# Optimization experiments

Hardware: AMD Instinct MI355X
Metric: run time of the kernel (lower is better)

The kernel has to match this reference:

```python
import jax, jax.numpy as jnp
import numpy as np
from jax import lax

B, C, O, H, W = 4, 96, 96, 128, 128
K = 3      # kernel size everywhere
D = 2      # dilation of dconv
KK = K * K


def conv2d(x, w, b, pad, dil=1):
    # x: [B,C,H,W], w: [O,C,K,K]
    y = lax.conv_general_dilated(
        x, w, window_strides=(1, 1), padding=[(pad, pad), (pad, pad)],
        rhs_dilation=(dil, dil), dimension_numbers=('NCHW', 'OIHW', 'NCHW'))
    return y + b[None, :, None, None]


def bilinear_sample(img, py, px):
    # img: [B,C,H,W]; py,px: [B,KK,H,W] float sample coords (zero outside)
    y0 = jnp.floor(py)
    x0 = jnp.floor(px)
    wy = py - y0
    wx = px - x0
    flat = img.reshape(B, 1, C, H * W)  # broadcast over KK

    def gather(yi, xi):
        valid = (yi >= 0) & (yi < H) & (xi >= 0) & (xi < W)
        yc = jnp.clip(yi, 0, H - 1).astype(jnp.int32)
        xc = jnp.clip(xi, 0, W - 1).astype(jnp.int32)
        idx = (yc * W + xc).reshape(B, KK, 1, H * W)
        g = jnp.take_along_axis(flat, idx, axis=3)  # [B,KK,C,H*W]
        g = g.reshape(B, KK, C, H, W)
        return g * valid.reshape(B, KK, 1, H, W)

    v00 = gather(y0, x0)
    v01 = gather(y0, x0 + 1)
    v10 = gather(y0 + 1, x0)
    v11 = gather(y0 + 1, x0 + 1)
    wy = wy[:, :, None]
    wx = wx[:, :, None]
    return ((1 - wy) * ((1 - wx) * v00 + wx * v01)
            + wy * ((1 - wx) * v10 + wx * v11))


def setup_inputs() -> dict:
    key = jax.random.key(0)
    ks = jax.random.split(key, 7)
    x = jax.random.normal(ks[0], (B, C, H, W), jnp.float32)
    s = 1.0 / np.sqrt(C * K * K)  # torch default conv init bound
    u = lambda k, shape: jax.random.uniform(k, shape, jnp.float32, -s, s)
    return dict(
        x=x,
        dconv_w=u(ks[1], (O, C, K, K)), dconv_b=u(ks[2], (O,)),
        off_w=u(ks[3], (2 * KK, C, K, K)), off_b=u(ks[4], (2 * KK,)),
        def_w=u(ks[5], (O, C, K, K)), def_b=u(ks[6], (O,)),
    )


def reference(x, dconv_w, dconv_b, off_w, off_b, def_w, def_b):
    # dilated conv + relu + residual (self.conv is unused in the original forward)
    x1 = conv2d(x, dconv_w, dconv_b, pad=D, dil=D)
    x3 = x + jax.nn.relu(x1)

    # offset prediction: [B, 2*KK, H, W] -> (dy, dx) per kernel tap
    offset = conv2d(x3, off_w, off_b, pad=1)
    off = offset.reshape(B, KK, 2, H, W)
    dy, dx = off[:, :, 0], off[:, :, 1]

    # base sampling grid: output pixel + kernel tap - padding
    ki, kj = jnp.meshgrid(jnp.arange(K), jnp.arange(K), indexing='ij')
    ky = (ki.reshape(-1) - (K - 1) // 2).astype(jnp.float32)  # [KK]
    kx = (kj.reshape(-1) - (K - 1) // 2).astype(jnp.float32)
    ygrid = jnp.arange(H, dtype=jnp.float32)[:, None]
    xgrid = jnp.arange(W, dtype=jnp.float32)[None, :]
    py = ygrid[None, None] + ky[None, :, None, None] + dy  # [B,KK,H,W]
    px = xgrid[None, None] + kx[None, :, None, None] + dx

    sampled = bilinear_sample(x3, py, px)  # [B,KK,C,H,W]
    out = jnp.einsum('bkchw,ock->bohw', sampled, def_w.reshape(O, C, KK))
    return out + def_b[None, :, None, None]
```

## Files before the change

### kernel.cpp

```cpp
#include <hip/hip_runtime.h>
#include <hip/hip_bf16.h>

#define BD 4
#define CD 96
#define OD 96
#define HD 128
#define WD 128
#define HWD (HD*WD)

typedef __attribute__((ext_vector_type(8))) short bfrag;
typedef __attribute__((ext_vector_type(4))) float ffrag;

__device__ __forceinline__ short f2bs(float f) {
    __hip_bfloat16 h = __float2bfloat16(f);
    return *reinterpret_cast<short*>(&h);
}

__device__ __forceinline__ int swizzle512(int gid) {
    return ((gid & 7) << 6) | (gid >> 3);
}

__global__ __launch_bounds__(256) void k_transpose(const float* __restrict__ x,
                                                   short* __restrict__ xb16) {
    __shared__ short tile[256 * 104];
    int pix0 = blockIdx.x * 256;
    int b = pix0 / HWD; int hw0 = pix0 % HWD;
    int tid = threadIdx.x;

    for (int e = tid; e < 96*64; e += 256) {
        int c = e >> 6, g = e & 63;
        float4 v = *(const float4*)(x + ((size_t)(b*96 + c))*HWD + hw0 + 4*g);
        tile[(4*g+0)*104 + c] = f2bs(v.x);
        tile[(4*g+1)*104 + c] = f2bs(v.y);
        tile[(4*g+2)*104 + c] = f2bs(v.z);
        tile[(4*g+3)*104 + c] = f2bs(v.w);
    }
    __syncthreads();
    for (int e = tid; e < 256*12; e += 256) {
        int px = e / 12, c8 = e % 12;
        bfrag v = *(const bfrag*)(tile + px*104 + c8*8);
        *(bfrag*)(xb16 + ((size_t)(pix0 + px))*96 + c8*8) = v;
    }
}

__global__ void k_repack(const float* __restrict__ dconv_w,
                         const float* __restrict__ off_w,
                         const float* __restrict__ def_w,
                         short* __restrict__ wB1,
                         short* __restrict__ wB2,
                         short* __restrict__ wB) {
    int t = blockIdx.x * blockDim.x + threadIdx.x;
    if (t < 27648) {
        int j = t & 7; int l = (t >> 3) & 63; int tile = t >> 9;
        int s = tile >> 1, nt = tile & 1;
        int k = 32*s + (l >> 4)*8 + j;
        int o = 16*nt + (l & 15);
        int c = k % 96, tap = k / 96;
        wB2[t] = (o < 18) ? f2bs(off_w[(o*96 + c)*9 + tap]) : (short)0;
    }
    if (t < 82944) {
        int j = t & 7; int l = (t >> 3) & 63; int tile = t >> 9;
        int s = tile / 6, nt = tile % 6;
        int k = 32*s + (l >> 4)*8 + j;
        int o = 16*nt + (l & 15);
        int c = k % 96, tap = k / 96;
        wB1[t] = f2bs(dconv_w[(o*96 + c)*9 + tap]);
        wB[t]  = f2bs(def_w [(o*96 + c)*9 + tap]);
    }
}

__global__ __launch_bounds__(256, 2) void k_conv1(const float* __restrict__ x,
                                                  const short* __restrict__ xb16,
                                                  const short* __restrict__ wB,
                                                  const float* __restrict__ bias,
                                                  short* __restrict__ x3b) {
    int pix0 = swizzle512(blockIdx.x) * 128;
    int b = pix0 / HWD; int hw0 = pix0 % HWD;
    int h = hw0 / WD;
    int tid = threadIdx.x;
    int l = tid & 63, wv = tid >> 6;
    int q = l >> 4, mr = l & 15;
    int wq = 32*wv;
    const short* xb = xb16 + ((size_t)b * HWD) * 96;
    const bfrag az = {0,0,0,0,0,0,0,0};

    ffrag acc[2][6];
    #pragma unroll
    for (int mt = 0; mt < 2; mt++)
        #pragma unroll
        for (int nt = 0; nt < 6; nt++) acc[mt][nt] = ffrag{0.f,0.f,0.f,0.f};

    #pragma unroll 1
    for (int tap = 0; tap < 9; tap++) {
        int y = h + (tap/3)*2 - 2;
        if ((unsigned)y >= HD) continue;
        const short* abase[2]; bool vx[2];
        #pragma unroll
        for (int mt = 0; mt < 2; mt++) {
            int xx = wq + 16*mt + mr + (tap%3)*2 - 2;
            int xxc = min(max(xx, 0), WD-1);
            vx[mt] = (unsigned)xx < WD;
            abase[mt] = xb + ((size_t)(y*WD + xxc))*96 + q*8;
        }
        #pragma unroll
        for (int sc = 0; sc < 3; sc++) {
            const short* wb = wB + ((size_t)((tap*3+sc)*6)*64 + l)*8;
            bfrag bb[6];
            #pragma unroll
            for (int nt = 0; nt < 6; nt++) bb[nt] = *(const bfrag*)(wb + nt*512);
            #pragma unroll
            for (int mt = 0; mt < 2; mt++) {
                bfrag a = *(const bfrag*)(abase[mt] + sc*32);
                if (!vx[mt]) a = az;
                #pragma unroll
                for (int nt = 0; nt < 6; nt++)
                    acc[mt][nt] = __builtin_amdgcn_mfma_f32_16x16x32_bf16(a, bb[nt], acc[mt][nt], 0, 0, 0);
            }
        }
    }

    #pragma unroll
    for (int mt = 0; mt < 2; mt++) {
        int hwb = hw0 + wq + 16*mt + q*4;
        #pragma unroll
        for (int nt = 0; nt < 6; nt++) {
            int o = 16*nt + mr;
            float bo = bias[o];
            float4 xr = *(const float4*)(x + ((size_t)(b*96 + o))*HWD + hwb);
            short* op = x3b + ((size_t)(b*HWD + hwb))*96 + o;
            op[0]   = f2bs(xr.x + fmaxf(acc[mt][nt][0] + bo, 0.f));
            op[96]  = f2bs(xr.y + fmaxf(acc[mt][nt][1] + bo, 0.f));
            op[192] = f2bs(xr.z + fmaxf(acc[mt][nt][2] + bo, 0.f));
            op[288] = f2bs(xr.w + fmaxf(acc[mt][nt][3] + bo, 0.f));
        }
    }
}

__global__ __launch_bounds__(256, 2) void k_deform(const short* __restrict__ x3b,
                                                   const short* __restrict__ wB2,
                                                   const float* __restrict__ off_b,
                                                   const short* __restrict__ wB,
                                                   const float* __restrict__ def_b,
                                                   float* __restrict__ out) {
    __shared__ float offsb[128][20];

    int pix0 = swizzle512(blockIdx.x) * 128;
    int b = pix0 / HWD; int hw0 = pix0 % HWD;
    int h = hw0 / WD;
    int tid = threadIdx.x;
    int l = tid & 63, wv = tid >> 6;
    int q = l >> 4, mr = l & 15;
    int wq = 32*wv;
    const short* xb = x3b + ((size_t)b * HWD) * 96;
    const bfrag az = {0,0,0,0,0,0,0,0};

    ffrag oa[2][2];
    #pragma unroll
    for (int mt = 0; mt < 2; mt++)
        #pragma unroll
        for (int nt = 0; nt < 2; nt++) oa[mt][nt] = ffrag{0.f,0.f,0.f,0.f};

    #pragma unroll 1
    for (int tap = 0; tap < 9; tap++) {
        int y = h + tap/3 - 1;
        if ((unsigned)y >= HD) continue;
        const short* abase[2]; bool vx[2];
        #pragma unroll
        for (int mt = 0; mt < 2; mt++) {
            int xx = wq + 16*mt + mr + tap%3 - 1;
            int xxc = min(max(xx, 0), WD-1);
            vx[mt] = (unsigned)xx < WD;
            abase[mt] = xb + ((size_t)(y*WD + xxc))*96 + q*8;
        }
        #pragma unroll
        for (int sc = 0; sc < 3; sc++) {
            const short* wb = wB2 + ((size_t)((tap*3+sc)*2)*64 + l)*8;
            bfrag b0 = *(const bfrag*)(wb);
            bfrag b1 = *(const bfrag*)(wb + 512);
            #pragma unroll
            for (int mt = 0; mt < 2; mt++) {
                bfrag a = *(const bfrag*)(abase[mt] + sc*32);
                if (!vx[mt]) a = az;
                oa[mt][0] = __builtin_amdgcn_mfma_f32_16x16x32_bf16(a, b0, oa[mt][0], 0, 0, 0);
                oa[mt][1] = __builtin_amdgcn_mfma_f32_16x16x32_bf16(a, b1, oa[mt][1], 0, 0, 0);
            }
        }
    }
    #pragma unroll
    for (int mt = 0; mt < 2; mt++) {
        int row = wq + 16*mt + q*4;
        float bo0 = off_b[mr];
        #pragma unroll
        for (int r = 0; r < 4; r++) offsb[row + r][mr] = oa[mt][0][r] + bo0;
        if (mr < 2) {
            float bo1 = off_b[16 + mr];
            #pragma unroll
            for (int r = 0; r < 4; r++) offsb[row + r][16 + mr] = oa[mt][1][r] + bo1;
        }
    }

    ffrag acc[2][6];
    #pragma unroll
    for (int mt = 0; mt < 2; mt++)
        #pragma unroll
        for (int nt = 0; nt < 6; nt++) acc[mt][nt] = ffrag{0.f,0.f,0.f,0.f};

    #pragma unroll 1
    for (int tap = 0; tap < 9; tap++) {
        const short* pp[2][4];
        float fb[2][4];
        #pragma unroll
        for (int mt = 0; mt < 2; mt++) {
            int w = wq + 16*mt + mr;
            float dy = offsb[w][2*tap];
            float dx = offsb[w][2*tap + 1];
            float py  = (float)(h + tap/3 - 1) + dy;
            float pxf = (float)(w + tap%3 - 1) + dx;
            float y0f = floorf(py), x0f = floorf(pxf);
            float wy = py - y0f, wx = pxf - x0f;
            int y0 = (int)y0f, x0 = (int)x0f;
            int y1 = y0 + 1, x1 = x0 + 1;
            bool vy0 = (unsigned)y0 < HD, vy1 = (unsigned)y1 < HD;
            bool vx0 = (unsigned)x0 < WD, vx1 = (unsigned)x1 < WD;
            fb[mt][0] = (vy0 && vx0) ? (1.f-wy)*(1.f-wx) : 0.f;
            fb[mt][1] = (vy0 && vx1) ? (1.f-wy)*wx       : 0.f;
            fb[mt][2] = (vy1 && vx0) ? wy*(1.f-wx)       : 0.f;
            fb[mt][3] = (vy1 && vx1) ? wy*wx             : 0.f;
            int yc0 = min(max(y0,0),HD-1), yc1 = min(max(y1,0),HD-1);
            int xc0 = min(max(x0,0),WD-1), xc1 = min(max(x1,0),WD-1);
            pp[mt][0] = xb + ((size_t)(yc0*WD + xc0))*96 + q*8;
            pp[mt][1] = xb + ((size_t)(yc0*WD + xc1))*96 + q*8;
            pp[mt][2] = xb + ((size_t)(yc1*WD + xc0))*96 + q*8;
            pp[mt][3] = xb + ((size_t)(yc1*WD + xc1))*96 + q*8;
        }
        #pragma unroll
        for (int sc = 0; sc < 3; sc++) {
            int s = tap*3 + sc;
            const short* wb = wB + ((size_t)(s*6)*64 + l)*8;
            bfrag bbf[6];
            #pragma unroll
            for (int nt = 0; nt < 6; nt++) bbf[nt] = *(const bfrag*)(wb + nt*512);
            #pragma unroll
            for (int mt = 0; mt < 2; mt++) {
                bfrag c00 = *(const bfrag*)(pp[mt][0] + sc*32);
                bfrag c01 = *(const bfrag*)(pp[mt][1] + sc*32);
                bfrag c10 = *(const bfrag*)(pp[mt][2] + sc*32);
                bfrag c11 = *(const bfrag*)(pp[mt][3] + sc*32);
                const int* i00 = (const int*)&c00;
                const int* i01 = (const int*)&c01;
                const int* i10 = (const int*)&c10;
                const int* i11 = (const int*)&c11;
                float f00 = fb[mt][0], f01 = fb[mt][1];
                float f10 = fb[mt][2], f11 = fb[mt][3];
                int ap[4];
                #pragma unroll
                for (int d = 0; d < 4; d++) {
                    float a0 = __int_as_float(((unsigned)i00[d]) << 16);
                    float b0f = __int_as_float(((unsigned)i01[d]) << 16);
                    float c0f = __int_as_float(((unsigned)i10[d]) << 16);
                    float d0 = __int_as_float(((unsigned)i11[d]) << 16);
                    float a1 = __int_as_float(i00[d] & 0xffff0000);
                    float b1f = __int_as_float(i01[d] & 0xffff0000);
                    float c1f = __int_as_float(i10[d] & 0xffff0000);
                    float d1 = __int_as_float(i11[d] & 0xffff0000);
                    float rlo = f00*a0 + f01*b0f + f10*c0f + f11*d0;
                    float rhi = f00*a1 + f01*b1f + f10*c1f + f11*d1;
                    ap[d] = (int)((unsigned short)f2bs(rlo)) |
                            ((int)((unsigned short)f2bs(rhi)) << 16);
                }
                bfrag a = *(const bfrag*)ap;
                #pragma unroll
                for (int nt = 0; nt < 6; nt++)
                    acc[mt][nt] = __builtin_amdgcn_mfma_f32_16x16x32_bf16(a, bbf[nt], acc[mt][nt], 0, 0, 0);
            }
        }
    }

    #pragma unroll
    for (int mt = 0; mt < 2; mt++) {
        int hwb = hw0 + wq + 16*mt + q*4;
        #pragma unroll
        for (int nt = 0; nt < 6; nt++) {
            int o = 16*nt + mr;
            float bo = def_b[o];
            float4 v;
            v.x = acc[mt][nt][0] + bo; v.y = acc[mt][nt][1] + bo;
            v.z = acc[mt][nt][2] + bo; v.w = acc[mt][nt][3] + bo;
            *(float4*)(out + ((size_t)(b*96 + o))*HWD + hwb) = v;
        }
    }
}

extern "C" void kernel_launch(void* const* d_in, const int* in_sizes, int n_in,
                              void* d_out, int out_size, void* d_ws, size_t ws_size,
                              hipStream_t stream) {
    const float* x       = (const float*)d_in[0];
    const float* dconv_w = (const float*)d_in[1];
    const float* dconv_b = (const float*)d_in[2];
    const float* off_w   = (const float*)d_in[3];
    const float* off_b   = (const float*)d_in[4];
    const float* def_w   = (const float*)d_in[5];
    const float* def_b   = (const float*)d_in[6];
    float* out = (float*)d_out;

    char* ws = (char*)d_ws;
    short* xb16 = (short*)(ws);
    short* x3b  = (short*)(ws + 12582912);
    short* wB1  = (short*)(ws + 25165824);
    short* wB2  = (short*)(ws + 25331712);
    short* wB   = (short*)(ws + 25387008);

    k_repack<<<324, 256, 0, stream>>>(dconv_w, off_w, def_w, wB1, wB2, wB);
    k_transpose<<<(BD*HWD)/256, 256, 0, stream>>>(x, xb16);
    k_conv1<<<(BD*HWD)/128, 256, 0, stream>>>(x, xb16, wB1, dconv_b, x3b);
    k_deform<<<(BD*HWD)/128, 256, 0, stream>>>(x3b, wB2, off_b, wB, def_b, out);
}
```

Baseline: 173.7 us.

## Software-pipeline gathers and weight loads in conv kernels; merge prep kernels

The tap/channel-chunk loops in the dilated-conv, offset-conv and deformable-conv stages are flattened into a single 27-step loop. It double-buffers the A fragments (including the four bilinear corners) and the B weight fragments, so loads for step s+1 are issued before the MFMAs of step s. Address and weight computation for the next tap is hoisted one step ahead. The transpose and weight-repack kernels are also merged into one launch. The pipelining raises register pressure and could lower occupancy under the 2-waves launch bound, and row-invalid taps are now computed with zeroed inputs instead of being skipped.

```diff
diff --git a/kernel.cpp b/kernel.cpp
--- a/kernel.cpp
+++ b/kernel.cpp
@@ -20,52 +20,52 @@
     return ((gid & 7) << 6) | (gid >> 3);
 }
 
-__global__ __launch_bounds__(256) void k_transpose(const float* __restrict__ x,
-                                                   short* __restrict__ xb16) {
+__global__ __launch_bounds__(256) void k_prep(const float* __restrict__ x,
+                                              const float* __restrict__ dconv_w,
+                                              const float* __restrict__ off_w,
+                                              const float* __restrict__ def_w,
+                                              short* __restrict__ xb16,
+                                              short* __restrict__ wB1,
+                                              short* __restrict__ wB2,
+                                              short* __restrict__ wB) {
     __shared__ short tile[256 * 104];
-    int pix0 = blockIdx.x * 256;
-    int b = pix0 / HWD; int hw0 = pix0 % HWD;
     int tid = threadIdx.x;
-
-    for (int e = tid; e < 96*64; e += 256) {
-        int c = e >> 6, g = e & 63;
-        float4 v = *(const float4*)(x + ((size_t)(b*96 + c))*HWD + hw0 + 4*g);
-        tile[(4*g+0)*104 + c] = f2bs(v.x);
-        tile[(4*g+1)*104 + c] = f2bs(v.y);
-        tile[(4*g+2)*104 + c] = f2bs(v.z);
-        tile[(4*g+3)*104 + c] = f2bs(v.w);
-    }
-    __syncthreads();
-    for (int e = tid; e < 256*12; e += 256) {
-        int px = e / 12, c8 = e % 12;
-        bfrag v = *(const bfrag*)(tile + px*104 + c8*8);
-        *(bfrag*)(xb16 + ((size_t)(pix0 + px))*96 + c8*8) = v;
-    }
-}
-
-__global__ void k_repack(const float* __restrict__ dconv_w,
-                         const float* __restrict__ off_w,
-                         const float* __restrict__ def_w,
-                         short* __restrict__ wB1,
-                         short* __restrict__ wB2,
-                         short* __restrict__ wB) {
-    int t = blockIdx.x * blockDim.x + threadIdx.x;
-    if (t < 27648) {
-        int j = t & 7; int l = (t >> 3) & 63; int tile = t >> 9;
-        int s = tile >> 1, nt = tile & 1;
-        int k = 32*s + (l >> 4)*8 + j;
-        int o = 16*nt + (l & 15);
-        int c = k % 96, tap = k / 96;
-        wB2[t] = (o < 18) ? f2bs(off_w[(o*96 + c)*9 + tap]) : (short)0;
-    }
-    if (t < 82944) {
-        int j = t & 7; int l = (t >> 3) & 63; int tile = t >> 9;
-        int s = tile / 6, nt = tile % 6;
-        int k = 32*s + (l >> 4)*8 + j;
-        int o = 16*nt + (l & 15);
-        int c = k % 96, tap = k / 96;
-        wB1[t] = f2bs(dconv_w[(o*96 + c)*9 + tap]);
-        wB[t]  = f2bs(def_w [(o*96 + c)*9 + tap]);
+    if (blockIdx.x < 256) {
+        int pix0 = blockIdx.x * 256;
+        int b = pix0 / HWD; int hw0 = pix0 % HWD;
+        for (int e = tid; e < 96*64; e += 256) {
+            int c = e >> 6, g = e & 63;
+            float4 v = *(const float4*)(x + ((size_t)(b*96 + c))*HWD + hw0 + 4*g);
+            tile[(4*g+0)*104 + c] = f2bs(v.x);
+            tile[(4*g+1)*104 + c] = f2bs(v.y);
+            tile[(4*g+2)*104 + c] = f2bs(v.z);
+            tile[(4*g+3)*104 + c] = f2bs(v.w);
+        }
+        __syncthreads();
+        for (int e = tid; e < 256*12; e += 256) {
+            int px = e / 12, c8 = e % 12;
+            bfrag v = *(const bfrag*)(tile + px*104 + c8*8);
+            *(bfrag*)(xb16 + ((size_t)(pix0 + px))*96 + c8*8) = v;
+        }
+    } else {
+        int t = (blockIdx.x - 256) * 256 + tid;
+        if (t < 27648) {
+            int j = t & 7; int l = (t >> 3) & 63; int tl = t >> 9;
+            int s = tl >> 1, nt = tl & 1;
+            int k = 32*s + (l >> 4)*8 + j;
+            int o = 16*nt + (l & 15);
+            int c = k % 96, tap = k / 96;
+            wB2[t] = (o < 18) ? f2bs(off_w[(o*96 + c)*9 + tap]) : (short)0;
+        }
+        if (t < 82944) {
+            int j = t & 7; int l = (t >> 3) & 63; int tl = t >> 9;
+            int s = tl / 6, nt = tl % 6;
+            int k = 32*s + (l >> 4)*8 + j;
+            int o = 16*nt + (l & 15);
+            int c = k % 96, tap = k / 96;
+            wB1[t] = f2bs(dconv_w[(o*96 + c)*9 + tap]);
+            wB[t]  = f2bs(def_w [(o*96 + c)*9 + tap]);
+        }
     }
 }
 
@@ -84,38 +84,64 @@
     const short* xb = xb16 + ((size_t)b * HWD) * 96;
     const bfrag az = {0,0,0,0,0,0,0,0};
 
+    auto aoff = [&](int tap, int mt, bool* vv) -> int {
+        int ty = tap/3, tx = tap - 3*(tap/3);
+        int y  = h + ty*2 - 2;
+        int xx = wq + 16*mt + mr + tx*2 - 2;
+        bool vy = (unsigned)y < HD, vx = (unsigned)xx < WD;
+        *vv = vy && vx;
+        int yc = min(max(y,0),HD-1), xc = min(max(xx,0),WD-1);
+        return (yc*WD + xc)*96 + q*8;
+    };
+
     ffrag acc[2][6];
     #pragma unroll
     for (int mt = 0; mt < 2; mt++)
         #pragma unroll
         for (int nt = 0; nt < 6; nt++) acc[mt][nt] = ffrag{0.f,0.f,0.f,0.f};
 
-    #pragma unroll 1
-    for (int tap = 0; tap < 9; tap++) {
-        int y = h + (tap/3)*2 - 2;
-        if ((unsigned)y >= HD) continue;
-        const short* abase[2]; bool vx[2];
+    int aoC[2], aoN[2]; bool vC[2], vN[2];
+    bfrag gA[2], gIn[2], bA[6], bIn[6];
+
+    #pragma unroll
+    for (int mt = 0; mt < 2; mt++) aoC[mt] = aoff(0, mt, &vC[mt]);
+    #pragma unroll
+    for (int mt = 0; mt < 2; mt++) gA[mt] = *(const bfrag*)(xb + aoC[mt]);
+    #pragma unroll
+    for (int nt = 0; nt < 6; nt++) bA[nt] = *(const bfrag*)(wB + ((size_t)nt*64 + l)*8);
+
+    #pragma unroll 3
+    for (int s = 0; s < 27; s++) {
+        int tap = s / 3, sc = s - 3*tap;
+        if (sc == 0) {
+            int tn = tap + 1; if (tn > 8) tn = 8;
+            #pragma unroll
+            for (int mt = 0; mt < 2; mt++) aoN[mt] = aoff(tn, mt, &vN[mt]);
+        }
         #pragma unroll
         for (int mt = 0; mt < 2; mt++) {
-            int xx = wq + 16*mt + mr + (tap%3)*2 - 2;
-            int xxc = min(max(xx, 0), WD-1);
-            vx[mt] = (unsigned)xx < WD;
-            abase[mt] = xb + ((size_t)(y*WD + xxc))*96 + q*8;
-        }
-        #pragma unroll
-        for (int sc = 0; sc < 3; sc++) {
-            const short* wb = wB + ((size_t)((tap*3+sc)*6)*64 + l)*8;
-            bfrag bb[6];
-            #pragma unroll
-            for (int nt = 0; nt < 6; nt++) bb[nt] = *(const bfrag*)(wb + nt*512);
-            #pragma unroll
-            for (int mt = 0; mt < 2; mt++) {
-                bfrag a = *(const bfrag*)(abase[mt] + sc*32);
-                if (!vx[mt]) a = az;
-                #pragma unroll
-                for (int nt = 0; nt < 6; nt++)
-                    acc[mt][nt] = __builtin_amdgcn_mfma_f32_16x16x32_bf16(a, bb[nt], acc[mt][nt], 0, 0, 0);
-            }
+            int off = (sc < 2) ? (aoC[mt] + (sc+1)*32) : aoN[mt];
+            gIn[mt] = *(const bfrag*)(xb + off);
+        }
+        int sn = s + 1; if (sn > 26) sn = 26;
+        #pragma unroll
+        for (int nt = 0; nt < 6; nt++)
+            bIn[nt] = *(const bfrag*)(wB + ((size_t)(sn*6 + nt)*64 + l)*8);
+        #pragma unroll
+        for (int mt = 0; mt < 2; mt++) {
+            bfrag a = gA[mt];
+            if (!vC[mt]) a = az;
+            #pragma unroll
+            for (int nt = 0; nt < 6; nt++)
+                acc[mt][nt] = __builtin_amdgcn_mfma_f32_16x16x32_bf16(a, bA[nt], acc[mt][nt], 0, 0, 0);
+        }
+        #pragma unroll
+        for (int mt = 0; mt < 2; mt++) gA[mt] = gIn[mt];
+        #pragma unroll
+        for (int nt = 0; nt < 6; nt++) bA[nt] = bIn[nt];
+        if (sc == 2) {
+            #pragma unroll
+            for (int mt = 0; mt < 2; mt++) { aoC[mt] = aoN[mt]; vC[mt] = vN[mt]; }
         }
     }
 
@@ -154,125 +180,194 @@
     const short* xb = x3b + ((size_t)b * HWD) * 96;
     const bfrag az = {0,0,0,0,0,0,0,0};
 
-    ffrag oa[2][2];
+    {
+        auto aoff2 = [&](int tap, int mt, bool* vv) -> int {
+            int ty = tap/3, tx = tap - 3*(tap/3);
+            int y  = h + ty - 1;
+            int xx = wq + 16*mt + mr + tx - 1;
+            bool vy = (unsigned)y < HD, vx = (unsigned)xx < WD;
+            *vv = vy && vx;
+            int yc = min(max(y,0),HD-1), xc = min(max(xx,0),WD-1);
+            return (yc*WD + xc)*96 + q*8;
+        };
+
+        ffrag oa[2][2];
+        #pragma unroll
+        for (int mt = 0; mt < 2; mt++)
+            #pragma unroll
+            for (int nt = 0; nt < 2; nt++) oa[mt][nt] = ffrag{0.f,0.f,0.f,0.f};
+
+        int aoC[2], aoN[2]; bool vC[2], vN[2];
+        bfrag gA[2], gIn[2], bA[2], bIn[2];
+
+        #pragma unroll
+        for (int mt = 0; mt < 2; mt++) aoC[mt] = aoff2(0, mt, &vC[mt]);
+        #pragma unroll
+        for (int mt = 0; mt < 2; mt++) gA[mt] = *(const bfrag*)(xb + aoC[mt]);
+        #pragma unroll
+        for (int nt = 0; nt < 2; nt++) bA[nt] = *(const bfrag*)(wB2 + ((size_t)nt*64 + l)*8);
+
+        #pragma unroll 3
+        for (int s = 0; s < 27; s++) {
+            int tap = s / 3, sc = s - 3*tap;
+            if (sc == 0) {
+                int tn = tap + 1; if (tn > 8) tn = 8;
+                #pragma unroll
+                for (int mt = 0; mt < 2; mt++) aoN[mt] = aoff2(tn, mt, &vN[mt]);
+            }
+            #pragma unroll
+            for (int mt = 0; mt < 2; mt++) {
+                int off = (sc < 2) ? (aoC[mt] + (sc+1)*32) : aoN[mt];
+                gIn[mt] = *(const bfrag*)(xb + off);
+            }
+            int sn = s + 1; if (sn > 26) sn = 26;
+            #pragma unroll
+            for (int nt = 0; nt < 2; nt++)
+                bIn[nt] = *(const bfrag*)(wB2 + ((size_t)(sn*2 + nt)*64 + l)*8);
+            #pragma unroll
+            for (int mt = 0; mt < 2; mt++) {
+                bfrag a = gA[mt];
+                if (!vC[mt]) a = az;
+                oa[mt][0] = __builtin_amdgcn_mfma_f32_16x16x32_bf16(a, bA[0], oa[mt][0], 0, 0, 0);
+                oa[mt][1] = __builtin_amdgcn_mfma_f32_16x16x32_bf16(a, bA[1], oa[mt][1], 0, 0, 0);
+            }
+            #pragma unroll
+            for (int mt = 0; mt < 2; mt++) gA[mt] = gIn[mt];
+            #pragma unroll
+            for (int nt = 0; nt < 2; nt++) bA[nt] = bIn[nt];
+            if (sc == 2) {
+                #pragma unroll
+                for (int mt = 0; mt < 2; mt++) { aoC[mt] = aoN[mt]; vC[mt] = vN[mt]; }
+            }
+        }
+        #pragma unroll
+        for (int mt = 0; mt < 2; mt++) {
+            int row = wq + 16*mt + q*4;
+            float bo0 = off_b[mr];
+            #pragma unroll
+            for (int r = 0; r < 4; r++) offsb[row + r][mr] = oa[mt][0][r] + bo0;
+            if (mr < 2) {
+                float bo1 = off_b[16 + mr];
+                #pragma unroll
+                for (int r = 0; r < 4; r++) offsb[row + r][16 + mr] = oa[mt][1][r] + bo1;
+            }
+        }
+    }
+
+    auto mkptr = [&](int tap, float dy, float dx, int wp, float* fo, int* oo) {
+        int ty = tap/3, tx = tap - 3*(tap/3);
+        float py  = (float)(h + ty - 1) + dy;
+        float pxf = (float)(wp + tx - 1) + dx;
+        float y0f = floorf(py), x0f = floorf(pxf);
+        float wy = py - y0f, wx = pxf - x0f;
+        int y0 = (int)y0f, x0 = (int)x0f;
+        int y1 = y0 + 1, x1 = x0 + 1;
+        bool vy0 = (unsigned)y0 < HD, vy1 = (unsigned)y1 < HD;
+        bool vx0 = (unsigned)x0 < WD, vx1 = (unsigned)x1 < WD;
+        fo[0] = (vy0 && vx0) ? (1.f-wy)*(1.f-wx) : 0.f;
+        fo[1] = (vy0 && vx1) ? (1.f-wy)*wx       : 0.f;
+        fo[2] = (vy1 && vx0) ? wy*(1.f-wx)       : 0.f;
+        fo[3] = (vy1 && vx1) ? wy*wx             : 0.f;
+        int yc0 = min(max(y0,0),HD-1), yc1 = min(max(y1,0),HD-1);
+        int xc0 = min(max(x0,0),WD-1), xc1 = min(max(x1,0),WD-1);
+        oo[0] = (yc0*WD + xc0)*96 + q*8;
+        oo[1] = (yc0*WD + xc1)*96 + q*8;
+        oo[2] = (yc1*WD + xc0)*96 + q*8;
+        oo[3] = (yc1*WD + xc1)*96 + q*8;
+    };
+
+    ffrag acc[2][6];
     #pragma unroll
     for (int mt = 0; mt < 2; mt++)
         #pragma unroll
-        for (int nt = 0; nt < 2; nt++) oa[mt][nt] = ffrag{0.f,0.f,0.f,0.f};
-
-    #pragma unroll 1
-    for (int tap = 0; tap < 9; tap++) {
-        int y = h + tap/3 - 1;
-        if ((unsigned)y >= HD) continue;
-        const short* abase[2]; bool vx[2];
+        for (int nt = 0; nt < 6; nt++) acc[mt][nt] = ffrag{0.f,0.f,0.f,0.f};
+
+    float fbv[2][4], fbn[2][4], dyn[2], dxn[2];
+    int po[2][4], pon[2][4];
+    bfrag g[2][4], gin[2][4], bA[6], bIn[6];
+
+    #pragma unroll
+    for (int mt = 0; mt < 2; mt++) {
+        int wp = wq + 16*mt + mr;
+        mkptr(0, offsb[wp][0], offsb[wp][1], wp, fbv[mt], po[mt]);
+    }
+    #pragma unroll
+    for (int mt = 0; mt < 2; mt++)
+        #pragma unroll
+        for (int c = 0; c < 4; c++) g[mt][c] = *(const bfrag*)(xb + po[mt][c]);
+    #pragma unroll
+    for (int nt = 0; nt < 6; nt++) bA[nt] = *(const bfrag*)(wB + ((size_t)nt*64 + l)*8);
+
+    #pragma unroll 3
+    for (int s = 0; s < 27; s++) {
+        int tap = s / 3, sc = s - 3*tap;
+        if (sc == 0) {
+            int tn = tap + 1; if (tn > 8) tn = 8;
+            #pragma unroll
+            for (int mt = 0; mt < 2; mt++) {
+                int wp = wq + 16*mt + mr;
+                dyn[mt] = offsb[wp][2*tn];
+                dxn[mt] = offsb[wp][2*tn + 1];
+            }
+        }
+        if (sc == 1) {
+            int tn = tap + 1; if (tn > 8) tn = 8;
+            #pragma unroll
+            for (int mt = 0; mt < 2; mt++)
+                mkptr(tn, dyn[mt], dxn[mt], wq + 16*mt + mr, fbn[mt], pon[mt]);
+        }
+        #pragma unroll
+        for (int mt = 0; mt < 2; mt++)
+            #pragma unroll
+            for (int c = 0; c < 4; c++) {
+                int off = (sc < 2) ? (po[mt][c] + (sc+1)*32) : pon[mt][c];
+                gin[mt][c] = *(const bfrag*)(xb + off);
+            }
+        int sn = s + 1; if (sn > 26) sn = 26;
+        #pragma unroll
+        for (int nt = 0; nt < 6; nt++)
+            bIn[nt] = *(const bfrag*)(wB + ((size_t)(sn*6 + nt)*64 + l)*8);
+
         #pragma unroll
         for (int mt = 0; mt < 2; mt++) {
-            int xx = wq + 16*mt + mr + tap%3 - 1;
-            int xxc = min(max(xx, 0), WD-1);
-            vx[mt] = (unsigned)xx < WD;
-            abase[mt] = xb + ((size_t)(y*WD + xxc))*96 + q*8;
-        }
-        #pragma unroll
-        for (int sc = 0; sc < 3; sc++) {
-            const short* wb = wB2 + ((size_t)((tap*3+sc)*2)*64 + l)*8;
-            bfrag b0 = *(const bfrag*)(wb);
-            bfrag b1 = *(const bfrag*)(wb + 512);
-            #pragma unroll
-            for (int mt = 0; mt < 2; mt++) {
-                bfrag a = *(const bfrag*)(abase[mt] + sc*32);
-                if (!vx[mt]) a = az;
-                oa[mt][0] = __builtin_amdgcn_mfma_f32_16x16x32_bf16(a, b0, oa[mt][0], 0, 0, 0);
-                oa[mt][1] = __builtin_amdgcn_mfma_f32_16x16x32_bf16(a, b1, oa[mt][1], 0, 0, 0);
-            }
-        }
-    }
-    #pragma unroll
-    for (int mt = 0; mt < 2; mt++) {
-        int row = wq + 16*mt + q*4;
-        float bo0 = off_b[mr];
-        #pragma unroll
-        for (int r = 0; r < 4; r++) offsb[row + r][mr] = oa[mt][0][r] + bo0;
-        if (mr < 2) {
-            float bo1 = off_b[16 + mr];
-            #pragma unroll
-            for (int r = 0; r < 4; r++) offsb[row + r][16 + mr] = oa[mt][1][r] + bo1;
-        }
-    }
-
-    ffrag acc[2][6];
-    #pragma unroll
-    for (int mt = 0; mt < 2; mt++)
-        #pragma unroll
-        for (int nt = 0; nt < 6; nt++) acc[mt][nt] = ffrag{0.f,0.f,0.f,0.f};
-
-    #pragma unroll 1
-    for (int tap = 0; tap < 9; tap++) {
-        const short* pp[2][4];
-        float fb[2][4];
-        #pragma unroll
-        for (int mt = 0; mt < 2; mt++) {
-            int w = wq + 16*mt + mr;
-            float dy = offsb[w][2*tap];
-            float dx = offsb[w][2*tap + 1];
-            float py  = (float)(h + tap/3 - 1) + dy;
-            float pxf = (float)(w + tap%3 - 1) + dx;
-            float y0f = floorf(py), x0f = floorf(pxf);
-            float wy = py - y0f, wx = pxf - x0f;
-            int y0 = (int)y0f, x0 = (int)x0f;
-            int y1 = y0 + 1, x1 = x0 + 1;
-            bool vy0 = (unsigned)y0 < HD, vy1 = (unsigned)y1 < HD;
-            bool vx0 = (unsigned)x0 < WD, vx1 = (unsigned)x1 < WD;
-            fb[mt][0] = (vy0 && vx0) ? (1.f-wy)*(1.f-wx) : 0.f;
-            fb[mt][1] = (vy0 && vx1) ? (1.f-wy)*wx       : 0.f;
-            fb[mt][2] = (vy1 && vx0) ? wy*(1.f-wx)       : 0.f;
-            fb[mt][3] = (vy1 && vx1) ? wy*wx             : 0.f;
-            int yc0 = min(max(y0,0),HD-1), yc1 = min(max(y1,0),HD-1);
-            int xc0 = min(max(x0,0),WD-1), xc1 = min(max(x1,0),WD-1);
-            pp[mt][0] = xb + ((size_t)(yc0*WD + xc0))*96 + q*8;
-            pp[mt][1] = xb + ((size_t)(yc0*WD + xc1))*96 + q*8;
-            pp[mt][2] = xb + ((size_t)(yc1*WD + xc0))*96 + q*8;
-            pp[mt][3] = xb + ((size_t)(yc1*WD + xc1))*96 + q*8;
-        }
-        #pragma unroll
-        for (int sc = 0; sc < 3; sc++) {
-            int s = tap*3 + sc;
-            const short* wb = wB + ((size_t)(s*6)*64 + l)*8;
-            bfrag bbf[6];
-            #pragma unroll
-            for (int nt = 0; nt < 6; nt++) bbf[nt] = *(const bfrag*)(wb + nt*512);
-            #pragma unroll
-            for (int mt = 0; mt < 2; mt++) {
-                bfrag c00 = *(const bfrag*)(pp[mt][0] + sc*32);
-                bfrag c01 = *(const bfrag*)(pp[mt][1] + sc*32);
-                bfrag c10 = *(const bfrag*)(pp[mt][2] + sc*32);
-                bfrag c11 = *(const bfrag*)(pp[mt][3] + sc*32);
-                const int* i00 = (const int*)&c00;
-                const int* i01 = (const int*)&c01;
-                const int* i10 = (const int*)&c10;
-                const int* i11 = (const int*)&c11;
-                float f00 = fb[mt][0], f01 = fb[mt][1];
-                float f10 = fb[mt][2], f11 = fb[mt][3];
-                int ap[4];
+            const int* i00 = (const int*)&g[mt][0];
+            const int* i01 = (const int*)&g[mt][1];
+            const int* i10 = (const int*)&g[mt][2];
+            const int* i11 = (const int*)&g[mt][3];
+            float f00 = fbv[mt][0], f01 = fbv[mt][1];
+            float f10 = fbv[mt][2], f11 = fbv[mt][3];
+            int ap[4];
+            #pragma unroll
+            for (int d = 0; d < 4; d++) {
+                float a0 = __int_as_float(((unsigned)i00[d]) << 16);
+                float b0f = __int_as_float(((unsigned)i01[d]) << 16);
+                float c0f = __int_as_float(((unsigned)i10[d]) << 16);
+                float d0 = __int_as_float(((unsigned)i11[d]) << 16);
+                float a1 = __int_as_float(i00[d] & 0xffff0000);
+                float b1f = __int_as_float(i01[d] & 0xffff0000);
+                float c1f = __int_as_float(i10[d] & 0xffff0000);
+                float d1 = __int_as_float(i11[d] & 0xffff0000);
+                float rlo = f00*a0 + f01*b0f + f10*c0f + f11*d0;
+                float rhi = f00*a1 + f01*b1f + f10*c1f + f11*d1;
+                ap[d] = (int)((unsigned short)f2bs(rlo)) |
+                        ((int)((unsigned short)f2bs(rhi)) << 16);
+            }
+            bfrag a = *(const bfrag*)ap;
+            #pragma unroll
+            for (int nt = 0; nt < 6; nt++)
+                acc[mt][nt] = __builtin_amdgcn_mfma_f32_16x16x32_bf16(a, bA[nt], acc[mt][nt], 0, 0, 0);
+        }
+        #pragma unroll
+        for (int mt = 0; mt < 2; mt++)
+            #pragma unroll
+            for (int c = 0; c < 4; c++) g[mt][c] = gin[mt][c];
+        #pragma unroll
+        for (int nt = 0; nt < 6; nt++) bA[nt] = bIn[nt];
+        if (sc == 2) {
+            #pragma unroll
+            for (int mt = 0; mt < 2; mt++)
                 #pragma unroll
-                for (int d = 0; d < 4; d++) {
-                    float a0 = __int_as_float(((unsigned)i00[d]) << 16);
-                    float b0f = __int_as_float(((unsigned)i01[d]) << 16);
-                    float c0f = __int_as_float(((unsigned)i10[d]) << 16);
-                    float d0 = __int_as_float(((unsigned)i11[d]) << 16);
-                    float a1 = __int_as_float(i00[d] & 0xffff0000);
-                    float b1f = __int_as_float(i01[d] & 0xffff0000);
-                    float c1f = __int_as_float(i10[d] & 0xffff0000);
-                    float d1 = __int_as_float(i11[d] & 0xffff0000);
-                    float rlo = f00*a0 + f01*b0f + f10*c0f + f11*d0;
-                    float rhi = f00*a1 + f01*b1f + f10*c1f + f11*d1;
-                    ap[d] = (int)((unsigned short)f2bs(rlo)) |
-                            ((int)((unsigned short)f2bs(rhi)) << 16);
-                }
-                bfrag a = *(const bfrag*)ap;
-                #pragma unroll
-                for (int nt = 0; nt < 6; nt++)
-                    acc[mt][nt] = __builtin_amdgcn_mfma_f32_16x16x32_bf16(a, bbf[nt], acc[mt][nt], 0, 0, 0);
-            }
+                for (int c = 0; c < 4; c++) { po[mt][c] = pon[mt][c]; fbv[mt][c] = fbn[mt][c]; }
         }
     }
 
@@ -310,8 +405,7 @@
     short* wB2  = (short*)(ws + 25331712);
     short* wB   = (short*)(ws + 25387008);
 
-    k_repack<<<324, 256, 0, stream>>>(dconv_w, off_w, def_w, wB1, wB2, wB);
-    k_transpose<<<(BD*HWD)/256, 256, 0, stream>>>(x, xb16);
+    k_prep<<<580, 256, 0, stream>>>(x, dconv_w, off_w, def_w, xb16, wB1, wB2, wB);
     k_conv1<<<(BD*HWD)/128, 256, 0, stream>>>(x, xb16, wB1, dconv_b, x3b);
     k_deform<<<(BD*HWD)/128, 256, 0, stream>>>(x3b, wB2, off_b, wB, def_b, out);
 }
```

After: 175.3 us. No clear change (+0.9%).

## Split taps across waves with LDS reduction and merge prep kernels

Applied to the files above, without the earlier changes.

Blocks now cover 64 pixels instead of 128, and the four waves are split into two pixel halves times two tap ranges (taps 0-4 and 5-8). Partial MFMA accumulators are reduced through shared memory before the epilogue, which doubles the grid and raises occupancy (launch bounds 4) to better hide gather and load latency. The transpose and weight-repack kernels are also merged into a single launch to save one kernel launch. In exchange it adds LDS traffic, extra barriers and an uneven 5/4 tap split between the two wave groups.

```diff
diff --git a/kernel.cpp b/kernel.cpp
--- a/kernel.cpp
+++ b/kernel.cpp
@@ -16,73 +16,79 @@
     return *reinterpret_cast<short*>(&h);
 }
 
-__device__ __forceinline__ int swizzle512(int gid) {
-    return ((gid & 7) << 6) | (gid >> 3);
-}
-
-__global__ __launch_bounds__(256) void k_transpose(const float* __restrict__ x,
-                                                   short* __restrict__ xb16) {
+__device__ __forceinline__ int swizzle1024(int gid) {
+    return ((gid & 7) << 7) | (gid >> 3);
+}
+
+__global__ __launch_bounds__(256) void k_prep(const float* __restrict__ x,
+                                              const float* __restrict__ dconv_w,
+                                              const float* __restrict__ off_w,
+                                              const float* __restrict__ def_w,
+                                              short* __restrict__ xb16,
+                                              short* __restrict__ wB1,
+                                              short* __restrict__ wB2,
+                                              short* __restrict__ wB) {
     __shared__ short tile[256 * 104];
-    int pix0 = blockIdx.x * 256;
-    int b = pix0 / HWD; int hw0 = pix0 % HWD;
     int tid = threadIdx.x;
-
-    for (int e = tid; e < 96*64; e += 256) {
-        int c = e >> 6, g = e & 63;
-        float4 v = *(const float4*)(x + ((size_t)(b*96 + c))*HWD + hw0 + 4*g);
-        tile[(4*g+0)*104 + c] = f2bs(v.x);
-        tile[(4*g+1)*104 + c] = f2bs(v.y);
-        tile[(4*g+2)*104 + c] = f2bs(v.z);
-        tile[(4*g+3)*104 + c] = f2bs(v.w);
-    }
-    __syncthreads();
-    for (int e = tid; e < 256*12; e += 256) {
-        int px = e / 12, c8 = e % 12;
-        bfrag v = *(const bfrag*)(tile + px*104 + c8*8);
-        *(bfrag*)(xb16 + ((size_t)(pix0 + px))*96 + c8*8) = v;
-    }
-}
-
-__global__ void k_repack(const float* __restrict__ dconv_w,
-                         const float* __restrict__ off_w,
-                         const float* __restrict__ def_w,
-                         short* __restrict__ wB1,
-                         short* __restrict__ wB2,
-                         short* __restrict__ wB) {
-    int t = blockIdx.x * blockDim.x + threadIdx.x;
-    if (t < 27648) {
-        int j = t & 7; int l = (t >> 3) & 63; int tile = t >> 9;
-        int s = tile >> 1, nt = tile & 1;
-        int k = 32*s + (l >> 4)*8 + j;
-        int o = 16*nt + (l & 15);
-        int c = k % 96, tap = k / 96;
-        wB2[t] = (o < 18) ? f2bs(off_w[(o*96 + c)*9 + tap]) : (short)0;
-    }
-    if (t < 82944) {
-        int j = t & 7; int l = (t >> 3) & 63; int tile = t >> 9;
-        int s = tile / 6, nt = tile % 6;
-        int k = 32*s + (l >> 4)*8 + j;
-        int o = 16*nt + (l & 15);
-        int c = k % 96, tap = k / 96;
-        wB1[t] = f2bs(dconv_w[(o*96 + c)*9 + tap]);
-        wB[t]  = f2bs(def_w [(o*96 + c)*9 + tap]);
-    }
-}
-
-__global__ __launch_bounds__(256, 2) void k_conv1(const float* __restrict__ x,
+    if (blockIdx.x < 256) {
+        int pix0 = blockIdx.x * 256;
+        int b = pix0 / HWD; int hw0 = pix0 % HWD;
+        for (int e = tid; e < 96*64; e += 256) {
+            int c = e >> 6, g = e & 63;
+            float4 v = *(const float4*)(x + ((size_t)(b*96 + c))*HWD + hw0 + 4*g);
+            tile[(4*g+0)*104 + c] = f2bs(v.x);
+            tile[(4*g+1)*104 + c] = f2bs(v.y);
+            tile[(4*g+2)*104 + c] = f2bs(v.z);
+            tile[(4*g+3)*104 + c] = f2bs(v.w);
+        }
+        __syncthreads();
+        for (int e = tid; e < 256*12; e += 256) {
+            int px = e / 12, c8 = e % 12;
+            bfrag v = *(const bfrag*)(tile + px*104 + c8*8);
+            *(bfrag*)(xb16 + ((size_t)(pix0 + px))*96 + c8*8) = v;
+        }
+    } else {
+        int t = (blockIdx.x - 256) * 256 + tid;
+        if (t < 27648) {
+            int j = t & 7; int l = (t >> 3) & 63; int tl = t >> 9;
+            int s = tl >> 1, nt = tl & 1;
+            int k = 32*s + (l >> 4)*8 + j;
+            int o = 16*nt + (l & 15);
+            int c = k % 96, tap = k / 96;
+            wB2[t] = (o < 18) ? f2bs(off_w[(o*96 + c)*9 + tap]) : (short)0;
+        }
+        if (t < 82944) {
+            int j = t & 7; int l = (t >> 3) & 63; int tl = t >> 9;
+            int s = tl / 6, nt = tl % 6;
+            int k = 32*s + (l >> 4)*8 + j;
+            int o = 16*nt + (l & 15);
+            int c = k % 96, tap = k / 96;
+            wB1[t] = f2bs(dconv_w[(o*96 + c)*9 + tap]);
+            wB[t]  = f2bs(def_w [(o*96 + c)*9 + tap]);
+        }
+    }
+}
+
+__global__ __launch_bounds__(256, 4) void k_conv1(const float* __restrict__ x,
                                                   const short* __restrict__ xb16,
                                                   const short* __restrict__ wB,
                                                   const float* __restrict__ bias,
                                                   short* __restrict__ x3b) {
-    int pix0 = swizzle512(blockIdx.x) * 128;
+    __shared__ float red[2][48][64];
+
+    int lb = swizzle1024(blockIdx.x);
+    int pix0 = lb * 64;
     int b = pix0 / HWD; int hw0 = pix0 % HWD;
-    int h = hw0 / WD;
+    int h = hw0 / WD, w0 = hw0 % WD;
     int tid = threadIdx.x;
     int l = tid & 63, wv = tid >> 6;
+    int wp = wv & 1, ks = wv >> 1;
     int q = l >> 4, mr = l & 15;
-    int wq = 32*wv;
+    int wq = w0 + 32*wp;
     const short* xb = xb16 + ((size_t)b * HWD) * 96;
     const bfrag az = {0,0,0,0,0,0,0,0};
+
+    int tap_lo = ks ? 5 : 0, tap_hi = ks ? 9 : 5;
 
     ffrag acc[2][6];
     #pragma unroll
@@ -90,8 +96,7 @@
         #pragma unroll
         for (int nt = 0; nt < 6; nt++) acc[mt][nt] = ffrag{0.f,0.f,0.f,0.f};
 
-    #pragma unroll 1
-    for (int tap = 0; tap < 9; tap++) {
+    for (int tap = tap_lo; tap < tap_hi; tap++) {
         int y = h + (tap/3)*2 - 2;
         if ((unsigned)y >= HD) continue;
         const short* abase[2]; bool vx[2];
@@ -119,40 +124,65 @@
         }
     }
 
-    #pragma unroll
-    for (int mt = 0; mt < 2; mt++) {
-        int hwb = hw0 + wq + 16*mt + q*4;
-        #pragma unroll
-        for (int nt = 0; nt < 6; nt++) {
-            int o = 16*nt + mr;
-            float bo = bias[o];
-            float4 xr = *(const float4*)(x + ((size_t)(b*96 + o))*HWD + hwb);
-            short* op = x3b + ((size_t)(b*HWD + hwb))*96 + o;
-            op[0]   = f2bs(xr.x + fmaxf(acc[mt][nt][0] + bo, 0.f));
-            op[96]  = f2bs(xr.y + fmaxf(acc[mt][nt][1] + bo, 0.f));
-            op[192] = f2bs(xr.z + fmaxf(acc[mt][nt][2] + bo, 0.f));
-            op[288] = f2bs(xr.w + fmaxf(acc[mt][nt][3] + bo, 0.f));
-        }
-    }
-}
-
-__global__ __launch_bounds__(256, 2) void k_deform(const short* __restrict__ x3b,
+    if (ks == 1) {
+        #pragma unroll
+        for (int mt = 0; mt < 2; mt++)
+            #pragma unroll
+            for (int nt = 0; nt < 6; nt++)
+                #pragma unroll
+                for (int r = 0; r < 4; r++)
+                    red[wp][mt*24 + nt*4 + r][l] = acc[mt][nt][r];
+    }
+    __syncthreads();
+    if (ks == 0) {
+        #pragma unroll
+        for (int mt = 0; mt < 2; mt++)
+            #pragma unroll
+            for (int nt = 0; nt < 6; nt++)
+                #pragma unroll
+                for (int r = 0; r < 4; r++)
+                    acc[mt][nt][r] += red[wp][mt*24 + nt*4 + r][l];
+
+        #pragma unroll
+        for (int mt = 0; mt < 2; mt++) {
+            int hwb = hw0 + 32*wp + 16*mt + q*4;
+            #pragma unroll
+            for (int nt = 0; nt < 6; nt++) {
+                int o = 16*nt + mr;
+                float bo = bias[o];
+                float4 xr = *(const float4*)(x + ((size_t)(b*96 + o))*HWD + hwb);
+                short* op = x3b + ((size_t)(b*HWD + hwb))*96 + o;
+                op[0]   = f2bs(xr.x + fmaxf(acc[mt][nt][0] + bo, 0.f));
+                op[96]  = f2bs(xr.y + fmaxf(acc[mt][nt][1] + bo, 0.f));
+                op[192] = f2bs(xr.z + fmaxf(acc[mt][nt][2] + bo, 0.f));
+                op[288] = f2bs(xr.w + fmaxf(acc[mt][nt][3] + bo, 0.f));
+            }
+        }
+    }
+}
+
+__global__ __launch_bounds__(256, 4) void k_deform(const short* __restrict__ x3b,
                                                    const short* __restrict__ wB2,
                                                    const float* __restrict__ off_b,
                                                    const short* __restrict__ wB,
                                                    const float* __restrict__ def_b,
                                                    float* __restrict__ out) {
-    __shared__ float offsb[128][20];
-
-    int pix0 = swizzle512(blockIdx.x) * 128;
+    __shared__ float offsb[64][20];
+    __shared__ float red[2][48][64];
+
+    int lb = swizzle1024(blockIdx.x);
+    int pix0 = lb * 64;
     int b = pix0 / HWD; int hw0 = pix0 % HWD;
-    int h = hw0 / WD;
+    int h = hw0 / WD, w0 = hw0 % WD;
     int tid = threadIdx.x;
     int l = tid & 63, wv = tid >> 6;
+    int wp = wv & 1, ks = wv >> 1;
     int q = l >> 4, mr = l & 15;
-    int wq = 32*wv;
+    int wq = w0 + 32*wp;
     const short* xb = x3b + ((size_t)b * HWD) * 96;
     const bfrag az = {0,0,0,0,0,0,0,0};
+
+    int tap_lo = ks ? 5 : 0, tap_hi = ks ? 9 : 5;
 
     ffrag oa[2][2];
     #pragma unroll
@@ -160,8 +190,7 @@
         #pragma unroll
         for (int nt = 0; nt < 2; nt++) oa[mt][nt] = ffrag{0.f,0.f,0.f,0.f};
 
-    #pragma unroll 1
-    for (int tap = 0; tap < 9; tap++) {
+    for (int tap = tap_lo; tap < tap_hi; tap++) {
         int y = h + tap/3 - 1;
         if ((unsigned)y >= HD) continue;
         const short* abase[2]; bool vx[2];
@@ -186,18 +215,37 @@
             }
         }
     }
-    #pragma unroll
-    for (int mt = 0; mt < 2; mt++) {
-        int row = wq + 16*mt + q*4;
-        float bo0 = off_b[mr];
-        #pragma unroll
-        for (int r = 0; r < 4; r++) offsb[row + r][mr] = oa[mt][0][r] + bo0;
-        if (mr < 2) {
-            float bo1 = off_b[16 + mr];
-            #pragma unroll
-            for (int r = 0; r < 4; r++) offsb[row + r][16 + mr] = oa[mt][1][r] + bo1;
-        }
-    }
+
+    if (ks == 1) {
+        #pragma unroll
+        for (int mt = 0; mt < 2; mt++)
+            #pragma unroll
+            for (int nt = 0; nt < 2; nt++)
+                #pragma unroll
+                for (int r = 0; r < 4; r++)
+                    red[wp][mt*8 + nt*4 + r][l] = oa[mt][nt][r];
+    }
+    __syncthreads();
+    if (ks == 0) {
+        #pragma unroll
+        for (int mt = 0; mt < 2; mt++) {
+            #pragma unroll
+            for (int nt = 0; nt < 2; nt++)
+                #pragma unroll
+                for (int r = 0; r < 4; r++)
+                    oa[mt][nt][r] += red[wp][mt*8 + nt*4 + r][l];
+            int row = 32*wp + 16*mt + q*4;
+            float bo0 = off_b[mr];
+            #pragma unroll
+            for (int r = 0; r < 4; r++) offsb[row + r][mr] = oa[mt][0][r] + bo0;
+            if (mr < 2) {
+                float bo1 = off_b[16 + mr];
+                #pragma unroll
+                for (int r = 0; r < 4; r++) offsb[row + r][16 + mr] = oa[mt][1][r] + bo1;
+            }
+        }
+    }
+    __syncthreads();
 
     ffrag acc[2][6];
     #pragma unroll
@@ -205,17 +253,17 @@
         #pragma unroll
         for (int nt = 0; nt < 6; nt++) acc[mt][nt] = ffrag{0.f,0.f,0.f,0.f};
 
-    #pragma unroll 1
-    for (int tap = 0; tap < 9; tap++) {
+    for (int tap = tap_lo; tap < tap_hi; tap++) {
         const short* pp[2][4];
         float fb[2][4];
         #pragma unroll
         for (int mt = 0; mt < 2; mt++) {
-            int w = wq + 16*mt + mr;
-            float dy = offsb[w][2*tap];
-            float dx = offsb[w][2*tap + 1];
+            int lpx = 32*wp + 16*mt + mr;
+            int wcol = w0 + lpx;
+            float dy = offsb[lpx][2*tap];
+            float dx = offsb[lpx][2*tap + 1];
             float py  = (float)(h + tap/3 - 1) + dy;
-            float pxf = (float)(w + tap%3 - 1) + dx;
+            float pxf = (float)(wcol + tap%3 - 1) + dx;
             float y0f = floorf(py), x0f = floorf(pxf);
             float wy = py - y0f, wx = pxf - x0f;
             int y0 = (int)y0f, x0 = (int)x0f;
@@ -235,8 +283,7 @@
         }
         #pragma unroll
         for (int sc = 0; sc < 3; sc++) {
-            int s = tap*3 + sc;
-            const short* wb = wB + ((size_t)(s*6)*64 + l)*8;
+            const short* wb = wB + ((size_t)((tap*3+sc)*6)*64 + l)*8;
             bfrag bbf[6];
             #pragma unroll
             for (int nt = 0; nt < 6; nt++) bbf[nt] = *(const bfrag*)(wb + nt*512);
@@ -276,17 +323,34 @@
         }
     }
 
-    #pragma unroll
-    for (int mt = 0; mt < 2; mt++) {
-        int hwb = hw0 + wq + 16*mt + q*4;
-        #pragma unroll
-        for (int nt = 0; nt < 6; nt++) {
-            int o = 16*nt + mr;
-            float bo = def_b[o];
-            float4 v;
-            v.x = acc[mt][nt][0] + bo; v.y = acc[mt][nt][1] + bo;
-            v.z = acc[mt][nt][2] + bo; v.w = acc[mt][nt][3] + bo;
-            *(float4*)(out + ((size_t)(b*96 + o))*HWD + hwb) = v;
+    if (ks == 1) {
+        #pragma unroll
+        for (int mt = 0; mt < 2; mt++)
+            #pragma unroll
+            for (int nt = 0; nt < 6; nt++)
+                #pragma unroll
+                for (int r = 0; r < 4; r++)
+                    red[wp][mt*24 + nt*4 + r][l] = acc[mt][nt][r];
+    }
+    __syncthreads();
+    if (ks == 0) {
+        #pragma unroll
+        for (int mt = 0; mt < 2; mt++) {
+            #pragma unroll
+            for (int nt = 0; nt < 6; nt++)
+                #pragma unroll
+                for (int r = 0; r < 4; r++)
+                    acc[mt][nt][r] += red[wp][mt*24 + nt*4 + r][l];
+            int hwb = hw0 + 32*wp + 16*mt + q*4;
+            #pragma unroll
+            for (int nt = 0; nt < 6; nt++) {
+                int o = 16*nt + mr;
+                float bo = def_b[o];
+                float4 v;
+                v.x = acc[mt][nt][0] + bo; v.y = acc[mt][nt][1] + bo;
+                v.z = acc[mt][nt][2] + bo; v.w = acc[mt][nt][3] + bo;
+                *(float4*)(out + ((size_t)(b*96 + o))*HWD + hwb) = v;
+            }
         }
     }
 }
@@ -310,8 +374,7 @@
     short* wB2  = (short*)(ws + 25331712);
     short* wB   = (short*)(ws + 25387008);
 
-    k_repack<<<324, 256, 0, stream>>>(dconv_w, off_w, def_w, wB1, wB2, wB);
-    k_transpose<<<(BD*HWD)/256, 256, 0, stream>>>(x, xb16);
-    k_conv1<<<(BD*HWD)/128, 256, 0, stream>>>(x, xb16, wB1, dconv_b, x3b);
-    k_deform<<<(BD*HWD)/128, 256, 0, stream>>>(x3b, wB2, off_b, wB, def_b, out);
-}
+    k_prep<<<580, 256, 0, stream>>>(x, dconv_w, off_w, def_w, xb16, wB1, wB2, wB);
+    k_conv1<<<(BD*HWD)/64, 256, 0, stream>>>(x, xb16, wB1, dconv_b, x3b);
+    k_deform<<<(BD*HWD)/64, 256, 0, stream>>>(x3b, wB2, off_b, wB, def_b, out);
+}
```

Result: slower. 287.6 us (+65.5%).
